# Kernel optimization log

Hardware: AMD Instinct MI355X
Metric: run time of the kernel (lower is better)

Reference implementation:

```python
import jax, jax.numpy as jnp
import numpy as np

N_NODES = 100000
N_EDGES = 1600000
NUM_FEATURES = 256
HIDDEN_DIM = 128
NUM_CLASSES = 16


def setup_inputs() -> dict:
    key = jax.random.key(0)
    k1, k2, k3, k4 = jax.random.split(key, 4)
    x = jax.random.normal(k1, (N_NODES, NUM_FEATURES), dtype=jnp.float32)
    edge_index = jax.random.randint(k2, (2, N_EDGES), 0, N_NODES, dtype=jnp.int64)
    # Glorot-style init like PyG GCNConv's Linear
    W1 = jax.random.normal(k3, (NUM_FEATURES, HIDDEN_DIM), dtype=jnp.float32) / np.sqrt(NUM_FEATURES)
    b1 = jnp.zeros((HIDDEN_DIM,), dtype=jnp.float32)
    W2 = jax.random.normal(k4, (HIDDEN_DIM, NUM_CLASSES), dtype=jnp.float32) / np.sqrt(HIDDEN_DIM)
    b2 = jnp.zeros((NUM_CLASSES,), dtype=jnp.float32)
    return {"x": x, "edge_index": edge_index, "W1": W1, "b1": b1, "W2": W2, "b2": b2}


def _gcn_norm(edge_index, num_nodes):
    """PyG GCNConv default: add self-loops, symmetric deg^{-1/2} A deg^{-1/2} norm."""
    loops = jnp.arange(num_nodes, dtype=edge_index.dtype)
    row = jnp.concatenate([edge_index[0], loops])  # source
    col = jnp.concatenate([edge_index[1], loops])  # target
    deg = jax.ops.segment_sum(jnp.ones_like(col, dtype=jnp.float32), col,
                              num_segments=num_nodes)
    dinv = jnp.where(deg > 0, jax.lax.rsqrt(deg), 0.0)
    norm = dinv[row] * dinv[col]  # [E + N]
    return row, col, norm


def _gcn_conv(h, row, col, norm, num_nodes):
    # transform first (PyG: lin then propagate), then normalized sum-aggregate
    msg = h[row] * norm[:, None]            # [E+N, d] gather + scale
    return jax.ops.segment_sum(msg, col, num_segments=num_nodes)


def reference(x, edge_index, W1, b1, W2, b2):
    num_nodes = x.shape[0]
    row, col, norm = _gcn_norm(edge_index, num_nodes)
    h = x @ W1
    h = _gcn_conv(h, row, col, norm, num_nodes) + b1
    h = jax.nn.relu(h)
    h = h @ W2
    out = _gcn_conv(h, row, col, norm, num_nodes) + b2
    return out
```

## Files before the change

kernel.cpp:

```cpp
#include <hip/hip_runtime.h>

#define N_NODES 100000
#define N_EDGES 1600000
#define F_IN    256
#define F_HID   128
#define F_OUT   16

#define BSHIFT  9
#define BNODES  512
#define NB      196
#define CHUNK   4096
#define NCHUNK  ((N_EDGES + CHUNK - 1) / CHUNK)

typedef __attribute__((ext_vector_type(8))) short short8;
typedef __attribute__((ext_vector_type(4))) float float4v;

__device__ __forceinline__ unsigned int bf16_rn(float f) {
    unsigned int u = __float_as_uint(f);
    return (u + 0x7FFFu + ((u >> 16) & 1u)) >> 16;
}
__device__ __forceinline__ unsigned int pk2(float lo, float hi) {
    return bf16_rn(lo) | (bf16_rn(hi) << 16);
}
__device__ __forceinline__ float blo(unsigned int u) { return __uint_as_float(u << 16); }
__device__ __forceinline__ float bhi(unsigned int u) { return __uint_as_float(u & 0xFFFF0000u); }


__global__ __launch_bounds__(256) void k_bhist(const int* __restrict__ coli,
                                               int* __restrict__ bcnt) {
    __shared__ int lc[NB];
    int tid = threadIdx.x;
    for (int i = tid; i < NB; i += 256) lc[i] = 0;
    __syncthreads();
    for (int e = blockIdx.x * 256 + tid; e < N_EDGES; e += 256 * 256)
        atomicAdd(&lc[coli[e] >> BSHIFT], 1);
    __syncthreads();
    for (int i = tid; i < NB; i += 256)
        if (lc[i]) atomicAdd(&bcnt[i], lc[i]);
}

__global__ __launch_bounds__(256) void k_bscan(const int* __restrict__ bcnt,
                                               int* __restrict__ bbase,
                                               int* __restrict__ bcur) {
    __shared__ int sc[256];
    int t = threadIdx.x;
    int v = (t < NB) ? bcnt[t] : 0;
    sc[t] = v; __syncthreads();
    for (int off = 1; off < 256; off <<= 1) {
        int x = (t >= off) ? sc[t - off] : 0;
        __syncthreads();
        sc[t] += x;
        __syncthreads();
    }
    if (t < NB) {
        int e = sc[t] - v;
        bbase[t] = e;
        bcur[t]  = e;
    }
    if (t == 0) bbase[NB] = N_EDGES;
}

__global__ __launch_bounds__(256) void k_binscatter(const int* __restrict__ rowi,
                                                    const int* __restrict__ coli,
                                                    int* __restrict__ bcur,
                                                    unsigned int* __restrict__ ebuf) {
    __shared__ int cnt[NB], gbase[NB], run[NB];
    int tid = threadIdx.x;
    int e0 = blockIdx.x * CHUNK;
    for (int i = tid; i < NB; i += 256) { cnt[i] = 0; run[i] = 0; }
    __syncthreads();
    int d[16], s[16];
    #pragma unroll
    for (int i = 0; i < 16; i++) {
        int e = e0 + i * 256 + tid;
        if (e < N_EDGES) {
            d[i] = coli[e]; s[i] = rowi[e];
            atomicAdd(&cnt[d[i] >> BSHIFT], 1);
        } else d[i] = -1;
    }
    __syncthreads();
    for (int i = tid; i < NB; i += 256)
        gbase[i] = cnt[i] ? atomicAdd(&bcur[i], cnt[i]) : 0;
    __syncthreads();
    #pragma unroll
    for (int i = 0; i < 16; i++) {
        if (d[i] >= 0) {
            int b = d[i] >> BSHIFT;
            int off = atomicAdd(&run[b], 1);
            ebuf[gbase[b] + off] = ((unsigned int)(d[i] & 511) << 17) | (unsigned int)s[i];
        }
    }
}

__global__ __launch_bounds__(256) void k_finalize(const int* __restrict__ bbase,
                                                  const unsigned int* __restrict__ ebuf,
                                                  int* __restrict__ row_ptr,
                                                  float* __restrict__ dinv,
                                                  int* __restrict__ esrc) {
    __shared__ int ndeg[BNODES];
    __shared__ int sc[BNODES];
    int tid = threadIdx.x;
    int b   = blockIdx.x;
    int nb0 = b << BSHIFT;
    int ebeg = bbase[b], eend = bbase[b + 1];
    ndeg[tid] = 0; ndeg[tid + 256] = 0;
    __syncthreads();
    for (int e = ebeg + tid; e < eend; e += 256)
        atomicAdd(&ndeg[ebuf[e] >> 17], 1);
    __syncthreads();
    int i0 = tid, i1 = tid + 256;
    sc[i0] = ndeg[i0]; sc[i1] = ndeg[i1];
    __syncthreads();
    for (int off = 1; off < BNODES; off <<= 1) {
        int v0 = (i0 >= off) ? sc[i0 - off] : 0;
        int v1 = (i1 >= off) ? sc[i1 - off] : 0;
        __syncthreads();
        sc[i0] += v0; sc[i1] += v1;
        __syncthreads();
    }
    #pragma unroll
    for (int k = 0; k < 2; k++) {
        int i = tid + k * 256;
        int n = nb0 + i;
        int deg = ndeg[i];
        int excl = sc[i] - deg;
        if (n < N_NODES) {
            row_ptr[n] = ebeg + excl;
            dinv[n]    = rsqrtf(1.0f + (float)deg);
        }
        ndeg[i] = excl;
    }
    if (b == NB - 1 && tid == 0) row_ptr[N_NODES] = N_EDGES;
    __syncthreads();
    for (int e = ebeg + tid; e < eend; e += 256) {
        unsigned int p = ebuf[e];
        int off = atomicAdd(&ndeg[p >> 17], 1);
        esrc[ebeg + off] = (int)(p & 0x1FFFFu);
    }
}


__global__ __launch_bounds__(256) void k_transW(const float* __restrict__ W1,
                                                ushort* __restrict__ Wt) {
    int t = blockIdx.x * 256 + threadIdx.x;
    int c = t & 127, k = t >> 7;
    Wt[c * 256 + k] = (ushort)bf16_rn(W1[k * 128 + c]);
}


__global__ __launch_bounds__(256) void k_gemm1(const float* __restrict__ x,
                                               const ushort* __restrict__ Wt,
                                               const float* __restrict__ dinv,
                                               ushort* __restrict__ g1) {
    __shared__ ushort Al[128 * 40];
    __shared__ ushort Bl[128 * 40];
    const int tid = threadIdx.x;
    const int w = tid >> 6;
    const int l = tid & 63;
    const int m = l & 15;
    const int q = l >> 4;
    const int R0 = blockIdx.x * 128;

    const int srow = tid >> 1;
    const int soff = (tid & 1) * 16;

    int vr = R0 + srow; if (vr > N_NODES - 1) vr = N_NODES - 1;
    const float*  xrow = &x[(size_t)vr * F_IN + soff];
    const ushort* wrow = &Wt[srow * 256 + soff];

    float4v acc[2][8];
    #pragma unroll
    for (int i = 0; i < 2; i++)
        #pragma unroll
        for (int j = 0; j < 8; j++) acc[i][j] = (float4v){0.f, 0.f, 0.f, 0.f};

    for (int kt = 0; kt < F_IN; kt += 32) {
        float4 f0 = *(const float4*)&xrow[kt + 0];
        float4 f1 = *(const float4*)&xrow[kt + 4];
        float4 f2 = *(const float4*)&xrow[kt + 8];
        float4 f3 = *(const float4*)&xrow[kt + 12];
        uint4 wv0 = *(const uint4*)&wrow[kt + 0];
        uint4 wv1 = *(const uint4*)&wrow[kt + 8];
        uint4 pa, pb;
        pa.x = pk2(f0.x, f0.y); pa.y = pk2(f0.z, f0.w);
        pa.z = pk2(f1.x, f1.y); pa.w = pk2(f1.z, f1.w);
        pb.x = pk2(f2.x, f2.y); pb.y = pk2(f2.z, f2.w);
        pb.z = pk2(f3.x, f3.y); pb.w = pk2(f3.z, f3.w);
        *(uint4*)&Al[srow * 40 + soff]     = pa;
        *(uint4*)&Al[srow * 40 + soff + 8] = pb;
        *(uint4*)&Bl[srow * 40 + soff]     = wv0;
        *(uint4*)&Bl[srow * 40 + soff + 8] = wv1;
        __syncthreads();

        short8 af0 = *(const short8*)&Al[(w * 32 + m) * 40 + q * 8];
        short8 af1 = *(const short8*)&Al[(w * 32 + 16 + m) * 40 + q * 8];
        #pragma unroll
        for (int n = 0; n < 8; n++) {
            short8 bfr = *(const short8*)&Bl[(n * 16 + m) * 40 + q * 8];
            acc[0][n] = __builtin_amdgcn_mfma_f32_16x16x32_bf16(af0, bfr, acc[0][n], 0, 0, 0);
            acc[1][n] = __builtin_amdgcn_mfma_f32_16x16x32_bf16(af1, bfr, acc[1][n], 0, 0, 0);
        }
        __syncthreads();
    }

    const int rbase = R0 + w * 32 + q * 4;
    float dv0[4], dv1[4];
    #pragma unroll
    for (int r = 0; r < 4; r++) {
        int v0 = rbase + r;      dv0[r] = (v0 < N_NODES) ? dinv[v0] : 0.f;
        int v1 = rbase + 16 + r; dv1[r] = (v1 < N_NODES) ? dinv[v1] : 0.f;
    }
    #pragma unroll
    for (int n = 0; n < 8; n++) {
        #pragma unroll
        for (int r = 0; r < 4; r++) {
            int v0 = rbase + r;
            if (v0 < N_NODES)
                g1[v0 * F_HID + n * 16 + m] = (ushort)bf16_rn(dv0[r] * acc[0][n][r]);
            int v1 = rbase + 16 + r;
            if (v1 < N_NODES)
                g1[v1 * F_HID + n * 16 + m] = (ushort)bf16_rn(dv1[r] * acc[1][n][r]);
        }
    }
}


__global__ __launch_bounds__(256) void k_agg1g2(const int* __restrict__ row_ptr,
                                                const int* __restrict__ esrc,
                                                const float* __restrict__ dinv,
                                                const unsigned int* __restrict__ g1,
                                                const float* __restrict__ b1,
                                                const float* __restrict__ W2,
                                                float* __restrict__ g2) {
    __shared__ float hl[4 * 132];
    __shared__ float W2s[F_HID * F_OUT];
    const int tid  = threadIdx.x;
    const int wave = tid >> 6;
    const int lane = tid & 63;
    const int node = blockIdx.x * 4 + wave;

    for (int i = tid; i < F_HID * F_OUT; i += 256) W2s[i] = W2[i];

    int s = row_ptr[node], t = row_ptr[node + 1];
    unsigned int u = g1[node * 64 + lane];
    float ax = blo(u), ay = bhi(u);
    int e = s;
    for (; e + 7 < t; e += 8) {
        int r0 = esrc[e],     r1 = esrc[e + 1], r2 = esrc[e + 2], r3 = esrc[e + 3];
        int r4 = esrc[e + 4], r5 = esrc[e + 5], r6 = esrc[e + 6], r7 = esrc[e + 7];
        unsigned int u0 = g1[r0 * 64 + lane], u1 = g1[r1 * 64 + lane];
        unsigned int u2 = g1[r2 * 64 + lane], u3 = g1[r3 * 64 + lane];
        unsigned int u4 = g1[r4 * 64 + lane], u5 = g1[r5 * 64 + lane];
        unsigned int u6 = g1[r6 * 64 + lane], u7 = g1[r7 * 64 + lane];
        ax += blo(u0) + blo(u1) + blo(u2) + blo(u3)
            + blo(u4) + blo(u5) + blo(u6) + blo(u7);
        ay += bhi(u0) + bhi(u1) + bhi(u2) + bhi(u3)
            + bhi(u4) + bhi(u5) + bhi(u6) + bhi(u7);
    }
    for (; e + 3 < t; e += 4) {
        int r0 = esrc[e], r1 = esrc[e + 1], r2 = esrc[e + 2], r3 = esrc[e + 3];
        unsigned int u0 = g1[r0 * 64 + lane], u1 = g1[r1 * 64 + lane];
        unsigned int u2 = g1[r2 * 64 + lane], u3 = g1[r3 * 64 + lane];
        ax += blo(u0) + blo(u1) + blo(u2) + blo(u3);
        ay += bhi(u0) + bhi(u1) + bhi(u2) + bhi(u3);
    }
    for (; e < t; e++) {
        unsigned int u0 = g1[esrc[e] * 64 + lane];
        ax += blo(u0); ay += bhi(u0);
    }
    float wv = dinv[node];
    float2 bb = ((const float2*)b1)[lane];
    hl[wave * 132 + lane * 2]     = fmaxf(fmaf(wv, ax, bb.x), 0.0f);
    hl[wave * 132 + lane * 2 + 1] = fmaxf(fmaf(wv, ay, bb.y), 0.0f);
    __syncthreads();

    const int col = lane & 15, part = lane >> 4;
    float acc = 0.f;
    #pragma unroll
    for (int i = 0; i < 32; i++) {
        int f = i * 4 + part;
        acc = fmaf(hl[wave * 132 + f], W2s[f * 16 + col], acc);
    }
    acc += __shfl_xor(acc, 16);
    acc += __shfl_xor(acc, 32);
    if (lane < 16) g2[node * 16 + col] = wv * acc;
}


__global__ __launch_bounds__(256) void k_agg2(const int* __restrict__ row_ptr,
                                              const int* __restrict__ esrc,
                                              const float* __restrict__ dinv,
                                              const float* __restrict__ g2,
                                              const float* __restrict__ b2,
                                              float* __restrict__ out) {
    int gid = blockIdx.x * 256 + threadIdx.x;
    int node = gid >> 4;
    int f = gid & 15;
    if (node >= N_NODES) return;
    int s = row_ptr[node], t = row_ptr[node + 1];
    float acc = g2[node * 16 + f];
    int e = s;
    for (; e + 7 < t; e += 8) {
        float a0 = g2[esrc[e] * 16 + f],     a1 = g2[esrc[e + 1] * 16 + f];
        float a2 = g2[esrc[e + 2] * 16 + f], a3 = g2[esrc[e + 3] * 16 + f];
        float a4 = g2[esrc[e + 4] * 16 + f], a5 = g2[esrc[e + 5] * 16 + f];
        float a6 = g2[esrc[e + 6] * 16 + f], a7 = g2[esrc[e + 7] * 16 + f];
        acc += a0 + a1 + a2 + a3 + a4 + a5 + a6 + a7;
    }
    for (; e + 3 < t; e += 4) {
        acc += g2[esrc[e] * 16 + f] + g2[esrc[e + 1] * 16 + f]
             + g2[esrc[e + 2] * 16 + f] + g2[esrc[e + 3] * 16 + f];
    }
    for (; e < t; e++) acc += g2[esrc[e] * 16 + f];
    out[node * 16 + f] = fmaf(dinv[node], acc, b2[f]);
}


extern "C" void kernel_launch(void* const* d_in, const int* in_sizes, int n_in,
                              void* d_out, int out_size, void* d_ws, size_t ws_size,
                              hipStream_t stream) {
    const float* x   = (const float*)d_in[0];
    const int*   ei  = (const int*)d_in[1];
    const float* W1  = (const float*)d_in[2];
    const float* b1  = (const float*)d_in[3];
    const float* W2  = (const float*)d_in[4];
    const float* b2  = (const float*)d_in[5];
    float* out = (float*)d_out;

    const int* rowi = ei;
    const int* coli = ei + N_EDGES;

    char* ws = (char*)d_ws;
    int*          bcnt    = (int*)(ws + 0);
    int*          bbase   = (int*)(ws + 4096);
    int*          bcur    = (int*)(ws + 8192);
    int*          row_ptr = (int*)(ws + 16384);
    float*        dinv    = (float*)(ws + 524288);
    unsigned int* ebuf    = (unsigned int*)(ws + 1048576);
    int*          esrc    = (int*)(ws + 8388608);
    ushort*       Wt      = (ushort*)(ws + 15728640);
    ushort*       g1      = (ushort*)(ws + 16777216);
    float*        g2      = (float*)(ws + 45088768);

    hipMemsetAsync(bcnt, 0, NB * sizeof(int), stream);

    k_bhist     <<<256, 256, 0, stream>>>(coli, bcnt);
    k_bscan     <<<1, 256, 0, stream>>>(bcnt, bbase, bcur);
    k_binscatter<<<NCHUNK, 256, 0, stream>>>(rowi, coli, bcur, ebuf);
    k_finalize  <<<NB, 256, 0, stream>>>(bbase, ebuf, row_ptr, dinv, esrc);
    k_transW    <<<128, 256, 0, stream>>>(W1, Wt);

    k_gemm1     <<<(N_NODES + 127) / 128, 256, 0, stream>>>(x, Wt, dinv, g1);
    k_agg1g2    <<<N_NODES / 4, 256, 0, stream>>>(row_ptr, esrc, dinv,
                                                  (const unsigned int*)g1, b1, W2, g2);
    k_agg2      <<<(N_NODES * 16 + 255) / 256, 256, 0, stream>>>(row_ptr, esrc, dinv, g2, b2, out);
}
```

Measured before the change: 371.5 us.

## Keep full W1 in swizzled LDS and load x fragments directly into registers

The GEMM1 kernel now stages all of transposed W1 (64 KB bf16) in shared memory once per block, using an XOR swizzle to avoid bank conflicts. Each lane loads and converts its own x rows straight into MFMA A-fragments, which removes the per-k-tile LDS staging of A and both __syncthreads. The cost is much higher LDS use per block, which lowers occupancy, and a redundant W1 load by every block. In agg1g2 the barrier moves to right after the W2 load, relying on the fact that each wave only reads its own hl row.

Result: faster. 358.7 us (-3.5%).

```diff
diff --git a/kernel.cpp b/kernel.cpp
--- a/kernel.cpp
+++ b/kernel.cpp
@@ -152,8 +152,7 @@
                                                const ushort* __restrict__ Wt,
                                                const float* __restrict__ dinv,
                                                ushort* __restrict__ g1) {
-    __shared__ ushort Al[128 * 40];
-    __shared__ ushort Bl[128 * 40];
+    __shared__ ushort Bl[128 * 256];
     const int tid = threadIdx.x;
     const int w = tid >> 6;
     const int l = tid & 63;
@@ -161,12 +160,23 @@
     const int q = l >> 4;
     const int R0 = blockIdx.x * 128;
 
-    const int srow = tid >> 1;
-    const int soff = (tid & 1) * 16;
-
-    int vr = R0 + srow; if (vr > N_NODES - 1) vr = N_NODES - 1;
-    const float*  xrow = &x[(size_t)vr * F_IN + soff];
-    const ushort* wrow = &Wt[srow * 256 + soff];
+    {
+        const uint4* Wg = (const uint4*)Wt;
+        uint4* Bl4 = (uint4*)Bl;
+        #pragma unroll
+        for (int it = 0; it < 16; it++) {
+            int i = it * 256 + tid;
+            int c = i >> 5, j = i & 31;
+            Bl4[c * 32 + (j ^ (c & 7))] = Wg[i];
+        }
+    }
+    __syncthreads();
+
+    int r0 = R0 + w * 32 + m;      if (r0 > N_NODES - 1) r0 = N_NODES - 1;
+    int r1 = R0 + w * 32 + 16 + m; if (r1 > N_NODES - 1) r1 = N_NODES - 1;
+    const float* xr0 = &x[(size_t)r0 * F_IN + q * 8];
+    const float* xr1 = &x[(size_t)r1 * F_IN + q * 8];
+    const short8* Bl8 = (const short8*)Bl;
 
     float4v acc[2][8];
     #pragma unroll
@@ -174,33 +184,25 @@
         #pragma unroll
         for (int j = 0; j < 8; j++) acc[i][j] = (float4v){0.f, 0.f, 0.f, 0.f};
 
+    #pragma unroll 2
     for (int kt = 0; kt < F_IN; kt += 32) {
-        float4 f0 = *(const float4*)&xrow[kt + 0];
-        float4 f1 = *(const float4*)&xrow[kt + 4];
-        float4 f2 = *(const float4*)&xrow[kt + 8];
-        float4 f3 = *(const float4*)&xrow[kt + 12];
-        uint4 wv0 = *(const uint4*)&wrow[kt + 0];
-        uint4 wv1 = *(const uint4*)&wrow[kt + 8];
-        uint4 pa, pb;
-        pa.x = pk2(f0.x, f0.y); pa.y = pk2(f0.z, f0.w);
-        pa.z = pk2(f1.x, f1.y); pa.w = pk2(f1.z, f1.w);
-        pb.x = pk2(f2.x, f2.y); pb.y = pk2(f2.z, f2.w);
-        pb.z = pk2(f3.x, f3.y); pb.w = pk2(f3.z, f3.w);
-        *(uint4*)&Al[srow * 40 + soff]     = pa;
-        *(uint4*)&Al[srow * 40 + soff + 8] = pb;
-        *(uint4*)&Bl[srow * 40 + soff]     = wv0;
-        *(uint4*)&Bl[srow * 40 + soff + 8] = wv1;
-        __syncthreads();
-
-        short8 af0 = *(const short8*)&Al[(w * 32 + m) * 40 + q * 8];
-        short8 af1 = *(const short8*)&Al[(w * 32 + 16 + m) * 40 + q * 8];
+        float4 a0 = *(const float4*)&xr0[kt];
+        float4 a1 = *(const float4*)&xr0[kt + 4];
+        float4 b0 = *(const float4*)&xr1[kt];
+        float4 b1 = *(const float4*)&xr1[kt + 4];
+        short8 af0, af1;
+        ((uint*)&af0)[0] = pk2(a0.x, a0.y); ((uint*)&af0)[1] = pk2(a0.z, a0.w);
+        ((uint*)&af0)[2] = pk2(a1.x, a1.y); ((uint*)&af0)[3] = pk2(a1.z, a1.w);
+        ((uint*)&af1)[0] = pk2(b0.x, b0.y); ((uint*)&af1)[1] = pk2(b0.z, b0.w);
+        ((uint*)&af1)[2] = pk2(b1.x, b1.y); ((uint*)&af1)[3] = pk2(b1.z, b1.w);
+        int jq = (kt >> 3) + q;
         #pragma unroll
         for (int n = 0; n < 8; n++) {
-            short8 bfr = *(const short8*)&Bl[(n * 16 + m) * 40 + q * 8];
+            int col = n * 16 + m;
+            short8 bfr = Bl8[col * 32 + (jq ^ (col & 7))];
             acc[0][n] = __builtin_amdgcn_mfma_f32_16x16x32_bf16(af0, bfr, acc[0][n], 0, 0, 0);
             acc[1][n] = __builtin_amdgcn_mfma_f32_16x16x32_bf16(af1, bfr, acc[1][n], 0, 0, 0);
         }
-        __syncthreads();
     }
 
     const int rbase = R0 + w * 32 + q * 4;
@@ -232,7 +234,7 @@
                                                 const float* __restrict__ b1,
                                                 const float* __restrict__ W2,
                                                 float* __restrict__ g2) {
-    __shared__ float hl[4 * 132];
+    __shared__ float hl[4][132];
     __shared__ float W2s[F_HID * F_OUT];
     const int tid  = threadIdx.x;
     const int wave = tid >> 6;
@@ -240,6 +242,7 @@
     const int node = blockIdx.x * 4 + wave;
 
     for (int i = tid; i < F_HID * F_OUT; i += 256) W2s[i] = W2[i];
+    __syncthreads();
 
     int s = row_ptr[node], t = row_ptr[node + 1];
     unsigned int u = g1[node * 64 + lane];
@@ -270,16 +273,15 @@
     }
     float wv = dinv[node];
     float2 bb = ((const float2*)b1)[lane];
-    hl[wave * 132 + lane * 2]     = fmaxf(fmaf(wv, ax, bb.x), 0.0f);
-    hl[wave * 132 + lane * 2 + 1] = fmaxf(fmaf(wv, ay, bb.y), 0.0f);
-    __syncthreads();
+    hl[wave][lane * 2]     = fmaxf(fmaf(wv, ax, bb.x), 0.0f);
+    hl[wave][lane * 2 + 1] = fmaxf(fmaf(wv, ay, bb.y), 0.0f);
 
     const int col = lane & 15, part = lane >> 4;
     float acc = 0.f;
     #pragma unroll
     for (int i = 0; i < 32; i++) {
         int f = i * 4 + part;
-        acc = fmaf(hl[wave * 132 + f], W2s[f * 16 + col], acc);
+        acc = fmaf(hl[wave][f], W2s[f * 16 + col], acc);
     }
     acc += __shfl_xor(acc, 16);
     acc += __shfl_xor(acc, 32);
```
